# Kernel tuning notes

Measured on AMD Instinct MI355X. Metric: run time of the kernel, lower is better.

Reference implementation:

```python
import jax, jax.numpy as jnp
import numpy as np

N = 80000   # active voxels
G = 64      # voxel grid side
K = 27      # 3x3x3 kernel taps


def _build_coord_maps():
    """Random unique voxel coords in a G^3 grid; 27-tap neighbor index map (-1 = missing)."""
    rng = np.random.default_rng(0)
    flat = rng.choice(G ** 3, size=N, replace=False).astype(np.int64)
    coords = np.stack(np.unravel_index(flat, (G, G, G)), axis=1)  # (N,3)
    order = np.argsort(flat)
    skeys = flat[order]
    offs = [(dx, dy, dz) for dx in (-1, 0, 1) for dy in (-1, 0, 1) for dz in (-1, 0, 1)]
    nbr = np.full((K, N), -1, np.int32)
    for k, (dx, dy, dz) in enumerate(offs):
        nc = coords + np.array([dx, dy, dz])
        inb = np.all((nc >= 0) & (nc < G), axis=1)
        nkey = nc[:, 0] * G * G + nc[:, 1] * G + nc[:, 2]
        pos = np.clip(np.searchsorted(skeys, nkey), 0, N - 1)
        hit = inb & (skeys[pos] == nkey)
        nbr[k] = np.where(hit, order[pos], -1)
    return nbr


_W_SPECS = [('a1w', (27, 96, 64)), ('a2w', (64, 64)), ('a3w', (27, 64, 64)), ('a4w', (64, 64)),
            ('b1w', (27, 256, 64)), ('b2w', (64, 64)), ('b3w', (27, 64, 32)), ('b4w', (32, 32)),
            ('c1w', (27, 96, 128)), ('c2w', (128, 128)), ('c3w', (128, 128))]
_BN_SPECS = [('a1', 64), ('a2', 64), ('a3', 64), ('a4', 64),
             ('b1', 64), ('b2', 64), ('b3', 32), ('b4', 32),
             ('c1', 128), ('c2', 128), ('c3', 128)]


def setup_inputs() -> dict:
    key = jax.random.key(0)
    ks = jax.random.split(key, 64)
    inp = {
        'feat3d': jax.random.normal(ks[0], (N, 96), jnp.float32),
        'feat2d': jax.random.normal(ks[1], (N, 256), jnp.float32),
    }
    i = 2
    for name, shp in _W_SPECS:
        fan = float(np.prod(shp[:-1]))
        inp[name] = jax.random.normal(ks[i], shp, jnp.float32) * (1.0 / np.sqrt(fan))
        i += 1
    for pre, c in _BN_SPECS:  # folded eval-mode BN: y = x*scale + shift
        inp[pre + 's'] = 1.0 + 0.1 * jax.random.normal(ks[i], (c,), jnp.float32)
        inp[pre + 'b'] = 0.1 * jax.random.normal(ks[i + 1], (c,), jnp.float32)
        i += 2
    inp['nbr_idx'] = jnp.asarray(_build_coord_maps())
    inp['align_idx'] = jnp.arange(N, dtype=jnp.int32)  # 2D/3D share coordinates -> exact match
    return inp


def _sconv(x, W, nbr):
    """Sparse 3x3x3 conv: per-tap masked gather + GEMM, accumulated (gather-GEMM-scatter)."""
    out = jnp.zeros((x.shape[0], W.shape[-1]), x.dtype)
    for k in range(W.shape[0]):
        idx = nbr[k]
        g = jnp.where((idx >= 0)[:, None], x[jnp.maximum(idx, 0)], 0.0)
        out = out + g @ W[k]
    return out


def _bnrelu(x, s, b):
    return jax.nn.relu(x * s + b)


def reference(feat3d, feat2d,
              a1w, a2w, a3w, a4w, b1w, b2w, b3w, b4w, c1w, c2w, c3w,
              a1s, a1b, a2s, a2b, a3s, a3b, a4s, a4b,
              b1s, b1b, b2s, b2b, b3s, b3b, b4s, b4b,
              c1s, c1b, c2s, c2b, c3s, c3b,
              nbr_idx, align_idx):
    # 3D branch: 96 -> 64 (dropout = identity in eval)
    x = _bnrelu(_sconv(feat3d, a1w, nbr_idx), a1s, a1b)
    x = _bnrelu(x @ a2w, a2s, a2b)
    x = _bnrelu(_sconv(x, a3w, nbr_idx), a3s, a3b)
    x3 = _bnrelu(x @ a4w, a4s, a4b)
    # 2D branch: 256 -> 32
    y = _bnrelu(_sconv(feat2d, b1w, nbr_idx), b1s, b1b)
    y = _bnrelu(y @ b2w, b2s, b2b)
    y = _bnrelu(_sconv(y, b3w, nbr_idx), b3s, b3b)
    y2 = _bnrelu(y @ b4w, b4s, b4b)
    # features_at_coordinates: exact-match gather at the 3D coords, NaN/Inf -> 0
    ya = y2[align_idx]
    ya = jnp.where(jnp.isfinite(ya), ya, 0.0)
    # fusion: concat 64+32=96 -> 128
    z = jnp.concatenate([x3, ya], axis=1)
    z = _bnrelu(_sconv(z, c1w, nbr_idx), c1s, c1b)
    z = _bnrelu(z @ c2w, c2s, c2b)
    z = _bnrelu(z @ c3w, c3s, c3b)
    return z
```

## Files before the change

kernel.cpp:

```cpp
#include <hip/hip_runtime.h>

typedef __bf16 bf16;
typedef __bf16 bf16x8 __attribute__((ext_vector_type(8)));
typedef __bf16 bf16x4 __attribute__((ext_vector_type(4)));
typedef float  f32x4  __attribute__((ext_vector_type(4)));

__global__ void f2b_kernel(const float* __restrict__ src, bf16* __restrict__ dst, int n4) {
    int i = blockIdx.x * 256 + threadIdx.x;
    if (i >= n4) return;
    float4 v = ((const float4*)src)[i];
    bf16x4 o = { (bf16)v.x, (bf16)v.y, (bf16)v.z, (bf16)v.w };
    ((bf16x4*)dst)[i] = o;
}

__global__ void swz_kernel(const float* __restrict__ W, bf16* __restrict__ Wf,
                           int cin, int cout, int total) {
    int e = blockIdx.x * 256 + threadIdx.x;
    if (e >= total) return;
    int per_tap = cin * cout;
    int tap = e / per_tap;
    int t2  = e - tap * per_tap;
    int ntc = cout >> 4;
    int s   = t2 / (ntc * 512);
    int r3  = t2 - s * (ntc * 512);
    int nt  = r3 >> 9;
    int L   = (r3 & 511) >> 3;
    int j   = r3 & 7;
    int k   = s * 32 + (L >> 4) * 8 + j;
    int col = nt * 16 + (L & 15);
    Wf[e] = (bf16)W[((size_t)tap * cin + k) * cout + col];
}

template<int CIN, int C1, int TAPS, int KTILE, int C2, int C3>
__global__ __launch_bounds__(256, 3) void layer_kernel(
    const bf16* __restrict__ X,
    const bf16* __restrict__ W1,
    const bf16* __restrict__ W2,
    const bf16* __restrict__ W3,
    const int*  __restrict__ nbr,
    const float* __restrict__ sc1, const float* __restrict__ sh1,
    const float* __restrict__ sc2, const float* __restrict__ sh2,
    const float* __restrict__ sc3, const float* __restrict__ sh3,
    bf16* __restrict__ Y, float* __restrict__ Yf,
    int ystride, int yoff, int n, int nblocks)
{
    constexpr int M    = 128;
    constexpr int NT1  = C1 / 16;
    constexpr int WR1  = 4;
    constexpr int WC1  = (NT1 >= 2) ? NT1 / 2 : 1;
    constexpr int KH   = CIN / KTILE;
    constexpr int KS   = KTILE / 32;
    constexpr int CH   = KTILE / 8;
    constexpr int SREG = KTILE / 16;
    constexpr int AST  = KTILE + 8;
    constexpr int ABUF = M * AST;
    constexpr int ABY  = 2 * ABUF * 2;
    constexpr int LS1  = C1 + 8;
    constexpr int LS2  = C2 + 8;
    constexpr int L1BY = M * LS1 * 2;
    constexpr int L2BY = (C3 > 0) ? M * LS2 * 2 : 0;
    constexpr int SBY  = (ABY > L1BY ? (ABY > L2BY ? ABY : L2BY)
                                     : (L1BY > L2BY ? L1BY : L2BY));
    constexpr int NIT  = KH * TAPS;

    __shared__ __align__(16) char smem[SBY];
    __shared__ int idxs[TAPS * M];
    bf16* As = (bf16*)smem;

    const int tid = threadIdx.x;

    const int bq  = nblocks >> 3, br = nblocks & 7;
    const int bx  = blockIdx.x & 7, bs = blockIdx.x >> 3;
    const int sb  = bx * bq + (bx < br ? bx : br) + bs;
    const int base = sb * M;

    const int lane  = tid & 63;
    const int wv    = tid >> 6;
    const int m16   = lane & 15;
    const int quad  = lane >> 4;
    const int wrow1 = wv & 1;
    const int wcol1 = wv >> 1;

    for (int e = tid; e < TAPS * M; e += 256)
        idxs[e] = nbr[(e >> 7) * n + base + (e & (M - 1))];
    __syncthreads();

    int rr[SREG], cof[SREG], lofs[SREG];
#pragma unroll
    for (int j = 0; j < SREG; ++j) {
        int e = tid + 256 * j;
        rr[j]   = e / CH;
        int c   = e - rr[j] * CH;
        cof[j]  = c * 8;
        lofs[j] = rr[j] * AST + c * 8;
    }

    auto issue_loads = [&](int kh, int t, float4 (&sr)[SREG]) {
#pragma unroll
        for (int j = 0; j < SREG; ++j) {
            int idx = idxs[t * M + rr[j]];
            float4 val = {0.f, 0.f, 0.f, 0.f};
            if (idx >= 0) val = *(const float4*)(X + (size_t)idx * CIN + kh * KTILE + cof[j]);
            sr[j] = val;
        }
    };
    auto store_lds = [&](int buf, float4 (&sr)[SREG]) {
#pragma unroll
        for (int j = 0; j < SREG; ++j)
            *(float4*)(&As[buf * ABUF + lofs[j]]) = sr[j];
    };
    auto load_w = [&](int kh, int t, bf16x8 (&bw)[KS][WC1]) {
        const bf16* wt = W1 + (size_t)t * (CIN * C1);
#pragma unroll
        for (int s = 0; s < KS; ++s)
#pragma unroll
            for (int c = 0; c < WC1; ++c)
                bw[s][c] = *(const bf16x8*)(wt + ((kh * KS + s) * NT1 + wcol1 * WC1 + c) * 512 + lane * 8);
    };

    f32x4 acc1[WR1][WC1];
#pragma unroll
    for (int r = 0; r < WR1; ++r)
#pragma unroll
        for (int c = 0; c < WC1; ++c) acc1[r][c] = (f32x4){0.f, 0.f, 0.f, 0.f};

    auto mma_step = [&](int buf, bf16x8 (&bw)[KS][WC1]) {
#pragma unroll
        for (int s = 0; s < KS; ++s) {
            bf16x8 a[WR1];
#pragma unroll
            for (int r = 0; r < WR1; ++r)
                a[r] = *(const bf16x8*)(&As[buf * ABUF + ((wrow1 * WR1 + r) * 16 + m16) * AST + s * 32 + quad * 8]);
#pragma unroll
            for (int r = 0; r < WR1; ++r)
#pragma unroll
                for (int c = 0; c < WC1; ++c)
                    acc1[r][c] = __builtin_amdgcn_mfma_f32_16x16x32_bf16(a[r], bw[s][c], acc1[r][c], 0, 0, 0);
        }
    };

    float4 sregA[SREG], sregB[SREG];
    bf16x8 bfrA[KS][WC1], bfrB[KS][WC1];

    issue_loads(0, 0, sregA);
    load_w(0, 0, bfrA);
    store_lds(0, sregA);
    if (NIT > 1) issue_loads(0, 1, sregB);

    int ts = 2, khs = 0;
    int tw = 1, khw = 0;

    for (int it = 0; it < NIT; it += 2) {
        {
            __syncthreads();
            if (it + 1 < NIT) store_lds(1, sregB);
            if (it + 2 < NIT) {
                issue_loads(khs, ts, sregA);
                if (++ts == TAPS) { ts = 0; ++khs; }
            }
            if (it + 1 < NIT) {
                load_w(khw, tw, bfrB);
                if (++tw == TAPS) { tw = 0; ++khw; }
            }
            mma_step(0, bfrA);
        }
        if (it + 1 < NIT) {
            __syncthreads();
            if (it + 2 < NIT) store_lds(0, sregA);
            if (it + 3 < NIT) {
                issue_loads(khs, ts, sregB);
                if (++ts == TAPS) { ts = 0; ++khs; }
            }
            if (it + 2 < NIT) {
                load_w(khw, tw, bfrA);
                if (++tw == TAPS) { tw = 0; ++khw; }
            }
            mma_step(1, bfrB);
        }
    }

    __syncthreads();
    bf16* Lt1 = (bf16*)smem;
#pragma unroll
    for (int c = 0; c < WC1; ++c) {
        int col = (wcol1 * WC1 + c) * 16 + m16;
        float s1 = sc1[col], h1 = sh1[col];
#pragma unroll
        for (int r = 0; r < WR1; ++r) {
            int row0 = (wrow1 * WR1 + r) * 16 + quad * 4;
#pragma unroll
            for (int i = 0; i < 4; ++i) {
                float v = acc1[r][c][i] * s1 + h1;
                v = v > 0.f ? v : 0.f;
                Lt1[(row0 + i) * LS1 + col] = (bf16)v;
            }
        }
    }
    __syncthreads();

    constexpr int NT2 = C2 / 16;
    constexpr int WR2 = 4;
    constexpr int WC2 = (NT2 >= 2) ? NT2 / 2 : 1;
    constexpr int KS2 = C1 / 32;
    const int wrow2 = wv & 1, wcol2 = wv >> 1;

    f32x4 acc2[WR2][WC2];
#pragma unroll
    for (int r = 0; r < WR2; ++r)
#pragma unroll
        for (int c = 0; c < WC2; ++c) acc2[r][c] = (f32x4){0.f, 0.f, 0.f, 0.f};

#pragma unroll
    for (int s = 0; s < KS2; ++s) {
        bf16x8 a[WR2], bw[WC2];
#pragma unroll
        for (int r = 0; r < WR2; ++r)
            a[r] = *(const bf16x8*)(&Lt1[((wrow2 * WR2 + r) * 16 + m16) * LS1 + s * 32 + quad * 8]);
#pragma unroll
        for (int c = 0; c < WC2; ++c)
            bw[c] = *(const bf16x8*)(W2 + ((s * NT2 + wcol2 * WC2 + c) * 512 + lane * 8));
#pragma unroll
        for (int r = 0; r < WR2; ++r)
#pragma unroll
            for (int c = 0; c < WC2; ++c)
                acc2[r][c] = __builtin_amdgcn_mfma_f32_16x16x32_bf16(a[r], bw[c], acc2[r][c], 0, 0, 0);
    }

    if constexpr (C3 == 0) {
#pragma unroll
        for (int c = 0; c < WC2; ++c) {
            int col = (wcol2 * WC2 + c) * 16 + m16;
            float s2 = sc2[col], h2 = sh2[col];
#pragma unroll
            for (int r = 0; r < WR2; ++r) {
                int row0 = base + (wrow2 * WR2 + r) * 16 + quad * 4;
#pragma unroll
                for (int i = 0; i < 4; ++i) {
                    float v = acc2[r][c][i] * s2 + h2;
                    v = v > 0.f ? v : 0.f;
                    size_t off = (size_t)(row0 + i) * ystride + yoff + col;
                    if (Yf) Yf[off] = v;
                    else    Y[off] = (bf16)v;
                }
            }
        }
    } else {
        __syncthreads();
        bf16* Lt2 = (bf16*)smem;
#pragma unroll
        for (int c = 0; c < WC2; ++c) {
            int col = (wcol2 * WC2 + c) * 16 + m16;
            float s2 = sc2[col], h2 = sh2[col];
#pragma unroll
            for (int r = 0; r < WR2; ++r) {
                int row0 = (wrow2 * WR2 + r) * 16 + quad * 4;
#pragma unroll
                for (int i = 0; i < 4; ++i) {
                    float v = acc2[r][c][i] * s2 + h2;
                    v = v > 0.f ? v : 0.f;
                    Lt2[(row0 + i) * LS2 + col] = (bf16)v;
                }
            }
        }
        __syncthreads();

        constexpr int C3v = (C3 > 0) ? C3 : 16;
        constexpr int NT3 = C3v / 16;
        constexpr int WR3 = 4;
        constexpr int WC3 = (NT3 >= 2) ? NT3 / 2 : 1;
        constexpr int KS3 = C2 / 32;
        const int wrow3 = wv & 1, wcol3 = wv >> 1;

        f32x4 acc3[WR3][WC3];
#pragma unroll
        for (int r = 0; r < WR3; ++r)
#pragma unroll
            for (int c = 0; c < WC3; ++c) acc3[r][c] = (f32x4){0.f, 0.f, 0.f, 0.f};

#pragma unroll
        for (int s = 0; s < KS3; ++s) {
            bf16x8 a[WR3], bw[WC3];
#pragma unroll
            for (int r = 0; r < WR3; ++r)
                a[r] = *(const bf16x8*)(&Lt2[((wrow3 * WR3 + r) * 16 + m16) * LS2 + s * 32 + quad * 8]);
#pragma unroll
            for (int c = 0; c < WC3; ++c)
                bw[c] = *(const bf16x8*)(W3 + ((s * NT3 + wcol3 * WC3 + c) * 512 + lane * 8));
#pragma unroll
            for (int r = 0; r < WR3; ++r)
#pragma unroll
                for (int c = 0; c < WC3; ++c)
                    acc3[r][c] = __builtin_amdgcn_mfma_f32_16x16x32_bf16(a[r], bw[c], acc3[r][c], 0, 0, 0);
        }

#pragma unroll
        for (int c = 0; c < WC3; ++c) {
            int col = (wcol3 * WC3 + c) * 16 + m16;
            float s3 = sc3[col], h3 = sh3[col];
#pragma unroll
            for (int r = 0; r < WR3; ++r) {
                int row0 = base + (wrow3 * WR3 + r) * 16 + quad * 4;
#pragma unroll
                for (int i = 0; i < 4; ++i) {
                    float v = acc3[r][c][i] * s3 + h3;
                    v = v > 0.f ? v : 0.f;
                    size_t off = (size_t)(row0 + i) * ystride + yoff + col;
                    if (Yf) Yf[off] = v;
                    else    Y[off] = (bf16)v;
                }
            }
        }
    }
}

__global__ void concat_kernel(const bf16* __restrict__ y2, const int* __restrict__ align,
                              bf16* __restrict__ z, int n) {
    int e = blockIdx.x * 256 + threadIdx.x;
    if (e >= n * 32) return;
    int i = e >> 5, c = e & 31;
    int a = align[i];
    float v = (float)y2[(size_t)a * 32 + c];
    unsigned u = __builtin_bit_cast(unsigned, v);
    if ((u & 0x7f800000u) == 0x7f800000u) v = 0.f;
    z[(size_t)i * 96 + 64 + c] = (bf16)v;
}

extern "C" void kernel_launch(void* const* d_in, const int* in_sizes, int n_in,
                              void* d_out, int out_size, void* d_ws, size_t ws_size,
                              hipStream_t stream) {
    const float* feat3d = (const float*)d_in[0];
    const float* feat2d = (const float*)d_in[1];
    const float* Wsrc[11];
    for (int i = 0; i < 11; ++i) Wsrc[i] = (const float*)d_in[2 + i];
    const float* bn[22];
    for (int i = 0; i < 22; ++i) bn[i] = (const float*)d_in[13 + i];
    const int* nbr   = (const int*)d_in[35];
    const int* align = (const int*)d_in[36];
    float* out = (float*)d_out;

    const int n = in_sizes[0] / 96;

    char* ws = (char*)d_ws;
    size_t off = 0;
    auto alloc = [&](size_t bytes) -> void* {
        void* p = ws + off;
        off = (off + bytes + 255) & ~(size_t)255;
        return p;
    };
    bf16* F3 = (bf16*)alloc((size_t)n * 96 * 2);
    bf16* F2 = (bf16*)alloc((size_t)n * 256 * 2);
    static const int wt_taps[11] = {27, 1, 27, 1, 27, 1, 27, 1, 27, 1, 1};
    static const int wt_cin[11]  = {96, 64, 64, 64, 256, 64, 64, 32, 96, 128, 128};
    static const int wt_cout[11] = {64, 64, 64, 64, 64, 64, 32, 32, 128, 128, 128};
    bf16* Wf[11];
    for (int i = 0; i < 11; ++i)
        Wf[i] = (bf16*)alloc((size_t)wt_taps[i] * wt_cin[i] * wt_cout[i] * 2);
    bf16* tA = (bf16*)alloc((size_t)n * 64 * 2);
    bf16* tB = (bf16*)alloc((size_t)n * 64 * 2);
    bf16* y2 = (bf16*)alloc((size_t)n * 32 * 2);
    bf16* z  = (bf16*)alloc((size_t)n * 96 * 2);

    f2b_kernel<<<(n * 96 / 4 + 255) / 256, 256, 0, stream>>>(feat3d, F3, n * 96 / 4);
    f2b_kernel<<<(n * 256 / 4 + 255) / 256, 256, 0, stream>>>(feat2d, F2, n * 256 / 4);
    for (int i = 0; i < 11; ++i) {
        int total = wt_taps[i] * wt_cin[i] * wt_cout[i];
        swz_kernel<<<(total + 255) / 256, 256, 0, stream>>>(Wsrc[i], Wf[i], wt_cin[i], wt_cout[i], total);
    }

    const int GB = n / 128;

    layer_kernel<96, 64, 27, 32, 64, 0><<<GB, 256, 0, stream>>>(
        F3, Wf[0], Wf[1], nullptr, nbr,
        bn[0], bn[1], bn[2], bn[3], nullptr, nullptr,
        tB, nullptr, 64, 0, n, GB);
    layer_kernel<64, 64, 27, 64, 64, 0><<<GB, 256, 0, stream>>>(
        tB, Wf[2], Wf[3], nullptr, nbr,
        bn[4], bn[5], bn[6], bn[7], nullptr, nullptr,
        z, nullptr, 96, 0, n, GB);

    layer_kernel<256, 64, 27, 64, 64, 0><<<GB, 256, 0, stream>>>(
        F2, Wf[4], Wf[5], nullptr, nbr,
        bn[8], bn[9], bn[10], bn[11], nullptr, nullptr,
        tA, nullptr, 64, 0, n, GB);
    layer_kernel<64, 32, 27, 64, 32, 0><<<GB, 256, 0, stream>>>(
        tA, Wf[6], Wf[7], nullptr, nbr,
        bn[12], bn[13], bn[14], bn[15], nullptr, nullptr,
        y2, nullptr, 32, 0, n, GB);

    concat_kernel<<<(n * 32 + 255) / 256, 256, 0, stream>>>(y2, align, z, n);

    layer_kernel<96, 128, 27, 32, 128, 128><<<GB, 256, 0, stream>>>(
        z, Wf[8], Wf[9], Wf[10], nbr,
        bn[16], bn[17], bn[18], bn[19], bn[20], bn[21],
        nullptr, out, 128, 0, n, GB);
}
```

Baseline: 620.6 us.

## Single-buffer LDS pipeline with tunable prefetch depth and lighter barriers

Replaces the double-buffered LDS A tile with a single buffer guarded by two barriers per step. Those barriers are a custom macro that waits only on LDS traffic (lgkmcnt), so in-flight global loads are not drained. Register prefetch depth and weight prefetch now depend on tile size, and the 96-channel layers move from K-tile 32 to a single 96-wide tile. The intent is to cut LDS footprint to allow higher occupancy and to reduce the number of barrier iterations. The cost is an extra barrier per step and, for the 96-wide tiles, weight loads issued right before the MFMAs, which can expose their latency.

```diff
diff --git a/kernel.cpp b/kernel.cpp
--- a/kernel.cpp
+++ b/kernel.cpp
@@ -4,6 +4,8 @@
 typedef __bf16 bf16x8 __attribute__((ext_vector_type(8)));
 typedef __bf16 bf16x4 __attribute__((ext_vector_type(4)));
 typedef float  f32x4  __attribute__((ext_vector_type(4)));
+
+#define BAR_NODRAIN() asm volatile("s_waitcnt lgkmcnt(0)\ns_barrier" ::: "memory")
 
 __global__ void f2b_kernel(const float* __restrict__ src, bf16* __restrict__ dst, int n4) {
     int i = blockIdx.x * 256 + threadIdx.x;
@@ -54,7 +56,7 @@
     constexpr int SREG = KTILE / 16;
     constexpr int AST  = KTILE + 8;
     constexpr int ABUF = M * AST;
-    constexpr int ABY  = 2 * ABUF * 2;
+    constexpr int ABY  = ABUF * 2;
     constexpr int LS1  = C1 + 8;
     constexpr int LS2  = C2 + 8;
     constexpr int L1BY = M * LS1 * 2;
@@ -62,6 +64,8 @@
     constexpr int SBY  = (ABY > L1BY ? (ABY > L2BY ? ABY : L2BY)
                                      : (L1BY > L2BY ? L1BY : L2BY));
     constexpr int NIT  = KH * TAPS;
+    constexpr int D    = (SREG <= 4) ? 2 : 1;
+    constexpr bool WPRE = (KS * WC1 <= 4);
 
     __shared__ __align__(16) char smem[SBY];
     __shared__ int idxs[TAPS * M];
@@ -104,10 +108,10 @@
             sr[j] = val;
         }
     };
-    auto store_lds = [&](int buf, float4 (&sr)[SREG]) {
+    auto store_lds = [&](float4 (&sr)[SREG]) {
 #pragma unroll
         for (int j = 0; j < SREG; ++j)
-            *(float4*)(&As[buf * ABUF + lofs[j]]) = sr[j];
+            *(float4*)(&As[lofs[j]]) = sr[j];
     };
     auto load_w = [&](int kh, int t, bf16x8 (&bw)[KS][WC1]) {
         const bf16* wt = W1 + (size_t)t * (CIN * C1);
@@ -124,13 +128,13 @@
 #pragma unroll
         for (int c = 0; c < WC1; ++c) acc1[r][c] = (f32x4){0.f, 0.f, 0.f, 0.f};
 
-    auto mma_step = [&](int buf, bf16x8 (&bw)[KS][WC1]) {
+    auto mma_step = [&](bf16x8 (&bw)[KS][WC1]) {
 #pragma unroll
         for (int s = 0; s < KS; ++s) {
             bf16x8 a[WR1];
 #pragma unroll
             for (int r = 0; r < WR1; ++r)
-                a[r] = *(const bf16x8*)(&As[buf * ABUF + ((wrow1 * WR1 + r) * 16 + m16) * AST + s * 32 + quad * 8]);
+                a[r] = *(const bf16x8*)(&As[((wrow1 * WR1 + r) * 16 + m16) * AST + s * 32 + quad * 8]);
 #pragma unroll
             for (int r = 0; r < WR1; ++r)
 #pragma unroll
@@ -143,39 +147,46 @@
     bf16x8 bfrA[KS][WC1], bfrB[KS][WC1];
 
     issue_loads(0, 0, sregA);
-    load_w(0, 0, bfrA);
-    store_lds(0, sregA);
-    if (NIT > 1) issue_loads(0, 1, sregB);
-
-    int ts = 2, khs = 0;
-    int tw = 1, khw = 0;
+    if constexpr (D == 2) { if (NIT > 1) issue_loads(0, 1, sregB); }
+    if constexpr (WPRE) load_w(0, 0, bfrA);
+
+    int ts = D % TAPS, khs = D / TAPS;
+    int tw = WPRE ? 1 : 0, khw = 0;
 
     for (int it = 0; it < NIT; it += 2) {
         {
-            __syncthreads();
-            if (it + 1 < NIT) store_lds(1, sregB);
-            if (it + 2 < NIT) {
+            BAR_NODRAIN();
+            store_lds(sregA);
+            if (it + D < NIT) {
                 issue_loads(khs, ts, sregA);
                 if (++ts == TAPS) { ts = 0; ++khs; }
             }
-            if (it + 1 < NIT) {
-                load_w(khw, tw, bfrB);
-                if (++tw == TAPS) { tw = 0; ++khw; }
-            }
-            mma_step(0, bfrA);
-        }
-        if (it + 1 < NIT) {
-            __syncthreads();
-            if (it + 2 < NIT) store_lds(0, sregA);
-            if (it + 3 < NIT) {
-                issue_loads(khs, ts, sregB);
-                if (++ts == TAPS) { ts = 0; ++khs; }
-            }
-            if (it + 2 < NIT) {
+            BAR_NODRAIN();
+            if constexpr (WPRE) {
+                if (it + 1 < NIT) { load_w(khw, tw, bfrB); if (++tw == TAPS) { tw = 0; ++khw; } }
+            } else {
                 load_w(khw, tw, bfrA);
                 if (++tw == TAPS) { tw = 0; ++khw; }
             }
-            mma_step(1, bfrB);
+            mma_step(bfrA);
+        }
+        if (it + 1 < NIT) {
+            BAR_NODRAIN();
+            if constexpr (D == 2) store_lds(sregB); else store_lds(sregA);
+            if (it + 1 + D < NIT) {
+                if constexpr (D == 2) issue_loads(khs, ts, sregB);
+                else                  issue_loads(khs, ts, sregA);
+                if (++ts == TAPS) { ts = 0; ++khs; }
+            }
+            BAR_NODRAIN();
+            if constexpr (WPRE) {
+                if (it + 2 < NIT) { load_w(khw, tw, bfrA); if (++tw == TAPS) { tw = 0; ++khw; } }
+                mma_step(bfrB);
+            } else {
+                load_w(khw, tw, bfrA);
+                if (++tw == TAPS) { tw = 0; ++khw; }
+                mma_step(bfrA);
+            }
         }
     }
 
@@ -369,7 +380,7 @@
 
     const int GB = n / 128;
 
-    layer_kernel<96, 64, 27, 32, 64, 0><<<GB, 256, 0, stream>>>(
+    layer_kernel<96, 64, 27, 96, 64, 0><<<GB, 256, 0, stream>>>(
         F3, Wf[0], Wf[1], nullptr, nbr,
         bn[0], bn[1], bn[2], bn[3], nullptr, nullptr,
         tB, nullptr, 64, 0, n, GB);
@@ -389,7 +400,7 @@
 
     concat_kernel<<<(n * 32 + 255) / 256, 256, 0, stream>>>(y2, align, z, n);
 
-    layer_kernel<96, 128, 27, 32, 128, 128><<<GB, 256, 0, stream>>>(
+    layer_kernel<96, 128, 27, 96, 128, 128><<<GB, 256, 0, stream>>>(
         z, Wf[8], Wf[9], Wf[10], nbr,
         bn[16], bn[17], bn[18], bn[19], bn[20], bn[21],
         nullptr, out, 128, 0, n, GB);
```

Result: no change. 615.3 us (-0.9%).
